# Optimization experiments

Measured on AMD Instinct MI355X. Metric: run time of the kernel, lower is better.

Reference implementation:

```python
import jax, jax.numpy as jnp
import numpy as np

N, D = 8192, 4096  # D must be a power of 2 for FWHT


def fwht(x):
    """Unnormalized Fast Walsh-Hadamard Transform along the last axis (len = 2^k)."""
    orig_shape = x.shape
    d = orig_shape[-1]
    x = x.reshape(-1, d)
    h = 1
    while h < d:
        x = x.reshape(-1, d // (2 * h), 2, h)
        a = x[..., 0, :]
        b = x[..., 1, :]
        x = jnp.stack([a + b, a - b], axis=-2)
        h *= 2
    return x.reshape(orig_shape)


def setup_inputs() -> dict:
    key = jax.random.key(0)
    k = jax.random.split(key, 6)
    return {
        "x": jax.random.normal(k[0], (N, D), dtype=jnp.float32),
        "s1": jax.random.normal(k[1], (D,), dtype=jnp.float32),
        "s2": jax.random.normal(k[2], (D,), dtype=jnp.float32),
        "g_mu": jax.random.normal(k[3], (D,), dtype=jnp.float32),
        "g_rho": jax.random.normal(k[4], (D,), dtype=jnpp.float32) if False else jax.random.normal(k[4], (D,), dtype=jnp.float32),
        "epsilon": jax.random.normal(k[5], (D,), dtype=jnp.float32),
    }


def reference(x, s1, s2, g_mu, g_rho, epsilon):
    # W(u) = diag(s1) H diag(u) H diag(s2); forward (sample=True):
    #   b = x @ W(g_mu).T + x @ W(softplus(g_rho) * epsilon).T
    # Per-row (H symmetric): x @ W(u).T = s1 * fwht(u * fwht(s2 * x)).
    t = fwht(x * s2)                                  # [N, D], shared between both terms
    g_noise = jax.nn.softplus(g_rho) * epsilon        # g_sigma_sqrt @ epsilon
    b = s1 * fwht(t * g_mu) + s1 * fwht(t * g_noise)  # [N, D]
    return b
```

## Files before the change

### kernel.cpp

```cpp
#include <hip/hip_runtime.h>
#include <math.h>

#define D 4096
#define RPB 4

typedef float f4 __attribute__((ext_vector_type(4)));

__device__ __forceinline__ void wave_lds_fence() {
    __asm__ volatile("s_waitcnt lgkmcnt(0)" ::: "memory");
}

__device__ __forceinline__ void fwht64(float* v) {
#pragma unroll
    for (int h = 1; h < 64; h <<= 1) {
#pragma unroll
        for (int i = 0; i < 64; i += 2 * h) {
#pragma unroll
            for (int j = i; j < i + h; ++j) {
                const float a = v[j];
                const float b = v[j + h];
                v[j]     = a + b;
                v[j + h] = a - b;
            }
        }
    }
}

__global__ void whvi_prep(const float* __restrict__ g_mu,
                          const float* __restrict__ g_rho,
                          const float* __restrict__ eps,
                          float* __restrict__ gq) {
    const int i = blockIdx.x * 256 + threadIdx.x;
    const int l = i >> 6, k = i & 63;
    const int e = (l & 3) | (k << 2) | ((l >> 2) << 8);
    const float r  = g_rho[e];
    const float sp = (r > 20.f) ? r : log1pf(expf(r));
    gq[i] = g_mu[e] + sp * eps[e];
}

__global__ void __launch_bounds__(256) whvi_main(
    const float* __restrict__ x,  const float* __restrict__ s1,
    const float* __restrict__ s2, const float* __restrict__ gq,
    const float* __restrict__ g_mu, const float* __restrict__ g_rho,
    const float* __restrict__ eps, float* __restrict__ out) {
    __shared__ alignas(16) float lds_all[RPB][D];
    const int l = threadIdx.x & 63;
    const int w = threadIdx.x >> 6;
    float* lds = lds_all[w];
    const long long row = (long long)blockIdx.x * RPB + w;
    const float* xr = x + row * (long long)D;
    float v[64];

#pragma unroll
    for (int q = 0; q < 16; ++q) {
        const int base = (l << 2) + (q << 8);
        const f4 xv = *reinterpret_cast<const f4*>(xr + base);
        const f4 sv = *reinterpret_cast<const f4*>(s2 + base);
        v[4 * q + 0] = xv.x * sv.x;
        v[4 * q + 1] = xv.y * sv.y;
        v[4 * q + 2] = xv.z * sv.z;
        v[4 * q + 3] = xv.w * sv.w;
    }

    fwht64(v);

#pragma unroll
    for (int q = 0; q < 16; ++q) {
        const int addr = ((l ^ (q & 7)) << 2) + (q << 8);
        f4 t;
        t.x = v[4 * q + 0]; t.y = v[4 * q + 1];
        t.z = v[4 * q + 2]; t.w = v[4 * q + 3];
        *reinterpret_cast<f4*>(&lds[addr]) = t;
    }
    wave_lds_fence();
    {
        const int xb = (l & 3) | ((l >> 2) << 8);
        const int mk = (l >> 2) & 7;
#pragma unroll
        for (int k = 0; k < 64; ++k)
            v[k] = lds[xb + ((k ^ mk) << 2)];
    }

    fwht64(v);

    if (gq) {
#pragma unroll
        for (int m = 0; m < 16; ++m) {
            const f4 gv = *reinterpret_cast<const f4*>(gq + l * 64 + 4 * m);
            v[4 * m + 0] *= gv.x;
            v[4 * m + 1] *= gv.y;
            v[4 * m + 2] *= gv.z;
            v[4 * m + 3] *= gv.w;
        }
    } else {
#pragma unroll
        for (int k = 0; k < 64; ++k) {
            const int e = (l & 3) | (k << 2) | ((l >> 2) << 8);
            const float r  = g_rho[e];
            const float sp = (r > 20.f) ? r : log1pf(expf(r));
            v[k] *= g_mu[e] + sp * eps[e];
        }
    }

    fwht64(v);

    wave_lds_fence();
    {
        const int xb = (l & 3) | ((l >> 2) << 8);
        const int mk = (l >> 2) & 7;
#pragma unroll
        for (int k = 0; k < 64; ++k)
            lds[xb + ((k ^ mk) << 2)] = v[k];
    }
    wave_lds_fence();
#pragma unroll
    for (int q = 0; q < 16; ++q) {
        const int addr = ((l ^ (q & 7)) << 2) + (q << 8);
        const f4 t = *reinterpret_cast<const f4*>(&lds[addr]);
        v[4 * q + 0] = t.x;
        v[4 * q + 1] = t.y;
        v[4 * q + 2] = t.z;
        v[4 * q + 3] = t.w;
    }

    fwht64(v);

    float* outr = out + row * (long long)D;
#pragma unroll
    for (int q = 0; q < 16; ++q) {
        const int base = (l << 2) + (q << 8);
        const f4 sv = *reinterpret_cast<const f4*>(s1 + base);
        f4 o;
        o.x = v[4 * q + 0] * sv.x;
        o.y = v[4 * q + 1] * sv.y;
        o.z = v[4 * q + 2] * sv.z;
        o.w = v[4 * q + 3] * sv.w;
        __builtin_nontemporal_store(o, reinterpret_cast<f4*>(outr + base));
    }
}

extern "C" void kernel_launch(void* const* d_in, const int* in_sizes, int n_in,
                              void* d_out, int out_size, void* d_ws, size_t ws_size,
                              hipStream_t stream) {
    const float* x     = (const float*)d_in[0];
    const float* s1    = (const float*)d_in[1];
    const float* s2    = (const float*)d_in[2];
    const float* g_mu  = (const float*)d_in[3];
    const float* g_rho = (const float*)d_in[4];
    const float* eps   = (const float*)d_in[5];
    float* out = (float*)d_out;
    const int rows = in_sizes[0] / D;

    float* gq = nullptr;
    if (ws_size >= (size_t)D * sizeof(float)) {
        gq = (float*)d_ws;
        whvi_prep<<<D / 256, 256, 0, stream>>>(g_mu, g_rho, eps, gq);
    }
    whvi_main<<<rows / RPB, 256, 0, stream>>>(x, s1, s2, gq, g_mu, g_rho, eps, out);
}
```

Measured before the change: 261.9 us.

## Use padded-stride LDS transpose with smaller 128-thread blocks

Replaces the XOR-swizzled LDS transpose with a padded layout (row stride 68 floats). Elements are written as scalars by row and read back as float4 by column, with the reverse pattern for the second transpose. The kernel now processes 2 rows per 128-thread block with launch bounds requesting 4 blocks per CU, which cuts LDS use per block and may let more waves be resident. It also splits the x load from the s2 multiply and replaces the nontemporal output store with a normal store, which may change cache behaviour for the large output.

```diff
diff --git a/kernel.cpp b/kernel.cpp
--- a/kernel.cpp
+++ b/kernel.cpp
@@ -2,7 +2,8 @@
 #include <math.h>
 
 #define D 4096
-#define RPB 4
+#define RPB 2
+#define STRIDE 68
 
 typedef float f4 __attribute__((ext_vector_type(4)));
 
@@ -38,12 +39,12 @@
     gq[i] = g_mu[e] + sp * eps[e];
 }
 
-__global__ void __launch_bounds__(256) whvi_main(
+__global__ void __launch_bounds__(128, 4) whvi_main(
     const float* __restrict__ x,  const float* __restrict__ s1,
     const float* __restrict__ s2, const float* __restrict__ gq,
     const float* __restrict__ g_mu, const float* __restrict__ g_rho,
     const float* __restrict__ eps, float* __restrict__ out) {
-    __shared__ alignas(16) float lds_all[RPB][D];
+    __shared__ alignas(16) float lds_all[RPB][64 * STRIDE];
     const int l = threadIdx.x & 63;
     const int w = threadIdx.x >> 6;
     float* lds = lds_all[w];
@@ -52,45 +53,40 @@
     float v[64];
 
 #pragma unroll
+    for (int q = 0; q < 16; ++q)
+        *reinterpret_cast<f4*>(&v[4 * q]) =
+            *reinterpret_cast<const f4*>(xr + (l << 2) + (q << 8));
+
+#pragma unroll
     for (int q = 0; q < 16; ++q) {
-        const int base = (l << 2) + (q << 8);
-        const f4 xv = *reinterpret_cast<const f4*>(xr + base);
-        const f4 sv = *reinterpret_cast<const f4*>(s2 + base);
-        v[4 * q + 0] = xv.x * sv.x;
-        v[4 * q + 1] = xv.y * sv.y;
-        v[4 * q + 2] = xv.z * sv.z;
-        v[4 * q + 3] = xv.w * sv.w;
+        const f4 s = *reinterpret_cast<const f4*>(s2 + (l << 2) + (q << 8));
+        v[4 * q + 0] *= s.x;
+        v[4 * q + 1] *= s.y;
+        v[4 * q + 2] *= s.z;
+        v[4 * q + 3] *= s.w;
     }
 
     fwht64(v);
 
 #pragma unroll
-    for (int q = 0; q < 16; ++q) {
-        const int addr = ((l ^ (q & 7)) << 2) + (q << 8);
-        f4 t;
-        t.x = v[4 * q + 0]; t.y = v[4 * q + 1];
-        t.z = v[4 * q + 2]; t.w = v[4 * q + 3];
-        *reinterpret_cast<f4*>(&lds[addr]) = t;
-    }
+    for (int r = 0; r < 64; ++r)
+        lds[r * STRIDE + l] = v[r];
     wave_lds_fence();
-    {
-        const int xb = (l & 3) | ((l >> 2) << 8);
-        const int mk = (l >> 2) & 7;
 #pragma unroll
-        for (int k = 0; k < 64; ++k)
-            v[k] = lds[xb + ((k ^ mk) << 2)];
-    }
+    for (int t = 0; t < 16; ++t)
+        *reinterpret_cast<f4*>(&v[4 * t]) =
+            *reinterpret_cast<const f4*>(&lds[l * STRIDE + 4 * t]);
 
     fwht64(v);
 
     if (gq) {
 #pragma unroll
-        for (int m = 0; m < 16; ++m) {
-            const f4 gv = *reinterpret_cast<const f4*>(gq + l * 64 + 4 * m);
-            v[4 * m + 0] *= gv.x;
-            v[4 * m + 1] *= gv.y;
-            v[4 * m + 2] *= gv.z;
-            v[4 * m + 3] *= gv.w;
+        for (int t = 0; t < 16; ++t) {
+            const f4 g = *reinterpret_cast<const f4*>(gq + (l << 6) + (t << 2));
+            v[4 * t + 0] *= g.x;
+            v[4 * t + 1] *= g.y;
+            v[4 * t + 2] *= g.z;
+            v[4 * t + 3] *= g.w;
         }
     } else {
 #pragma unroll
@@ -105,37 +101,27 @@
     fwht64(v);
 
     wave_lds_fence();
-    {
-        const int xb = (l & 3) | ((l >> 2) << 8);
-        const int mk = (l >> 2) & 7;
 #pragma unroll
-        for (int k = 0; k < 64; ++k)
-            lds[xb + ((k ^ mk) << 2)] = v[k];
-    }
+    for (int t = 0; t < 16; ++t)
+        *reinterpret_cast<f4*>(&lds[l * STRIDE + 4 * t]) =
+            *reinterpret_cast<const f4*>(&v[4 * t]);
     wave_lds_fence();
 #pragma unroll
-    for (int q = 0; q < 16; ++q) {
-        const int addr = ((l ^ (q & 7)) << 2) + (q << 8);
-        const f4 t = *reinterpret_cast<const f4*>(&lds[addr]);
-        v[4 * q + 0] = t.x;
-        v[4 * q + 1] = t.y;
-        v[4 * q + 2] = t.z;
-        v[4 * q + 3] = t.w;
-    }
+    for (int r = 0; r < 64; ++r)
+        v[r] = lds[r * STRIDE + l];
 
     fwht64(v);
 
     float* outr = out + row * (long long)D;
 #pragma unroll
     for (int q = 0; q < 16; ++q) {
-        const int base = (l << 2) + (q << 8);
-        const f4 sv = *reinterpret_cast<const f4*>(s1 + base);
+        const f4 s = *reinterpret_cast<const f4*>(s1 + (l << 2) + (q << 8));
         f4 o;
-        o.x = v[4 * q + 0] * sv.x;
-        o.y = v[4 * q + 1] * sv.y;
-        o.z = v[4 * q + 2] * sv.z;
-        o.w = v[4 * q + 3] * sv.w;
-        __builtin_nontemporal_store(o, reinterpret_cast<f4*>(outr + base));
+        o.x = v[4 * q + 0] * s.x;
+        o.y = v[4 * q + 1] * s.y;
+        o.z = v[4 * q + 2] * s.z;
+        o.w = v[4 * q + 3] * s.w;
+        *reinterpret_cast<f4*>(outr + (l << 2) + (q << 8)) = o;
     }
 }
 
@@ -156,5 +142,5 @@
         gq = (float*)d_ws;
         whvi_prep<<<D / 256, 256, 0, stream>>>(g_mu, g_rho, eps, gq);
     }
-    whvi_main<<<rows / RPB, 256, 0, stream>>>(x, s1, s2, gq, g_mu, g_rho, eps, out);
+    whvi_main<<<rows / RPB, 128, 0, stream>>>(x, s1, s2, gq, g_mu, g_rho, eps, out);
 }
```

New measurement: 254.9 us. 2.7% less time.
